# Kernel tuning notes

Measured on AMD Instinct MI355X. Metric: run time of the kernel, lower is better.

Reference implementation:

```python
import jax, jax.numpy as jnp
import numpy as np

NTAPS = 201
N_FWM = 2


def _dw_conv(x, w):
    # depthwise valid cross-correlation: x [N, C, L], w [C, 1, k] -> [N, C, L-k+1]
    return jax.lax.conv_general_dilated(x, w, (1,), 'VALID', feature_group_count=x.shape[1])


def _zcv(x, w):
    # ZcvFilter: x [B, L, Nm] real, w [k]; conv minus center-tap contribution
    B, L, Nm = x.shape
    k = w.shape[0]
    xr = jnp.transpose(x, (0, 2, 1)).reshape(B * Nm, 1, L)
    y = jax.lax.conv_general_dilated(xr, w.reshape(1, 1, k), (1,), 'VALID')
    ov = k - 1
    y = y - w[k // 2] * xr[:, :, ov // 2: L - ov // 2]
    return jnp.transpose(y.reshape(B, Nm, L - k + 1), (0, 2, 1))


def _fwm_filter(x, wr, wi):
    # FwmFilter: x complex [num, B, L, Nm]; depthwise complex conv over L per (num) channel
    num, B, L, Nm = x.shape
    k = wr.shape[-1]
    xp = jnp.transpose(x, (1, 3, 0, 2)).reshape(B * Nm, num, L)  # [B*Nm, num, L]
    yr = _dw_conv(xp.real, wr) - _dw_conv(xp.imag, wi)
    yi = _dw_conv(xp.real, wi) + _dw_conv(xp.imag, wr)
    y = (yr + 1j * yi).reshape(B, Nm, num, L - k + 1)
    return jnp.transpose(y, (2, 0, 3, 1))  # [num, B, L', Nm]


def setup_inputs() -> dict:
    key = jax.random.key(0)
    ks = jax.random.split(key, 8)
    B, M, Nm, k = 16, 40000, 2, NTAPS
    return {
        'x_real': jax.random.normal(ks[0], (B, M, Nm), jnp.float32),
        'x_imag': jax.random.normal(ks[1], (B, M, Nm), jnp.float32),
        'task_info': jax.random.uniform(ks[2], (B, 4), jnp.float32),  # col 0 = power in dBm
        'C00': (jax.random.normal(ks[3], (), jnp.float32) * 0.01),
        'ixpm_w': jax.random.normal(ks[4], (k,), jnp.float32) * 0.01,
        'icixpm_w': jax.random.normal(ks[5], (k,), jnp.float32) * 0.01,
        'fwm_wr': jax.random.normal(ks[6], (2 * N_FWM, 1, k), jnp.float32) * 0.01,
        'fwm_wi': jax.random.normal(ks[7], (2 * N_FWM, 1, k), jnp.float32) * 0.01,
        'i': 0,
    }


def reference(x_real, x_imag, task_info, C00, ixpm_w, icixpm_w, fwm_wr, fwm_wi, i):
    # share=True => module index min(i, 0) == 0; i unused beyond that
    del i
    Nm = x_real.shape[-1]
    t = NTAPS // 2
    P = 10.0 ** (task_info[:, 0] / 10.0) / Nm  # get_power
    sP = jnp.sqrt(P)[:, None, None]
    x = (x_real + 1j * x_imag) * sP  # [B, M, Nm] complex

    def trunc(a):
        return a[:, t:a.shape[1] - t]

    power = jnp.abs(x) ** 2
    ps = 2.0 * power + jnp.roll(power, 1, axis=-1)
    spm = C00 * jnp.sum(trunc(power), axis=-1, keepdims=True)
    ixpm = 2.0 * _zcv(ps, ixpm_w)
    phi = spm + ixpm  # [B, M-ntaps+1, Nm] real

    # FWM branch (n_fwm > 0)
    shifts = [s for s in range(-N_FWM, N_FWM + 1) if s != 0]
    ax = x
    ax_s = jnp.stack([jnp.roll(ax, s, axis=1) for s in shifts])  # [2n, B, M, Nm]
    ay = jnp.roll(x, 1, axis=-1)
    ay_s = jnp.roll(ax_s, 1, axis=-1)
    fwm_A = 2.0 * ax[None] * jnp.conj(ax_s) + ay[None] * jnp.conj(ay_s)
    fwm_B = ax[None] * jnp.conj(ay_s)
    fA = _fwm_filter(fwm_A, fwm_wr, fwm_wi)
    fB = _fwm_filter(fwm_B, fwm_wr, fwm_wi)
    fwm = jnp.sum(ax_s[:, :, t:-t] * fA, axis=0) + jnp.sum(ay_s[:, :, t:-t] * fB, axis=0)

    # icixpm branch
    q = x * jnp.roll(jnp.conj(x), 1, axis=-1)
    qc = _zcv(q.real, icixpm_w) + 1j * _zcv(q.imag, icixpm_w)
    ici = 1j * (jnp.roll(trunc(x), 1, axis=-1) * qc)

    out = trunc(x) * jnp.exp(1j * phi) + ici + fwm
    out = out / sP
    return jnp.stack([out.real, out.imag], axis=-1)  # [B, M-ntaps+1, Nm, 2]
```

## Files before the change

### kernel.cpp

```cpp
#include <hip/hip_runtime.h>
#include <math.h>

#define M_LEN 40000
#define B_SZ 16
#define K_TAPS 201
#define T_HALF 100
#define L_OUT 39800
#define TL 256
#define NTILES 156
#define NP 456
#define NPS 458
#define NPX 460
#define XSTR 464
#define SSTR 244
#define NSER 20
#define KT 7
#define NSLOT 68
#define NTHR 512

typedef unsigned int uint;
typedef unsigned short ushort_;
typedef __fp16 h2 __attribute__((ext_vector_type(2)));
typedef __fp16 h8 __attribute__((ext_vector_type(8)));
typedef float f4 __attribute__((ext_vector_type(4)));

static __device__ __forceinline__ float half_of(uint u, int hi) {
    ushort_ us = hi ? (ushort_)(u >> 16) : (ushort_)(u & 0xffffu);
    _Float16 h; __builtin_memcpy(&h, &us, 2); return (float)h;
}
static __device__ __forceinline__ uint pk2(float a, float b) {
    h2 h = __builtin_amdgcn_cvt_pkrtz(a, b);
    uint r; __builtin_memcpy(&r, &h, 4); return r;
}
static __device__ __forceinline__ h8 mk8(uint a, uint b, uint c, uint d) {
    uint uu[4] = {a, b, c, d}; h8 h; __builtin_memcpy(&h, uu, 16); return h;
}

__global__ void prep_weights(const float* __restrict__ wx, const float* __restrict__ wc,
                             const float* __restrict__ wr, const float* __restrict__ wi,
                             _Float16* __restrict__ Wb) {
    int idx = blockIdx.x * 256 + threadIdx.x;
    if (idx >= 16 * 224) return;
    int n = idx / 224, t = idx % 224;
    float f = 0.f;
    if (n == 0)      f = (t <= 200) ? wx[t] : 0.f;
    else if (n == 1) f = (t <= 200) ? wc[t] : 0.f;
    else if (n < 10) {
        int q = n - 2, sg = q >> 2, c = q & 3;
        if (c < 2) {
            f = (t <= 200) ? ((c == 1) ? wi : wr)[(2 + sg) * K_TAPS + t] : 0.f;
        } else {
            int tt = t - (sg + 1);
            f = (tt >= 0 && tt <= 200) ? ((c == 3) ? wi : wr)[(1 - sg) * K_TAPS + tt] : 0.f;
        }
    }
    Wb[idx] = (_Float16)f;
}

static __device__ __forceinline__ void calc_series(
        const _Float16 (*sxr)[XSTR], const _Float16 (*sxi)[XSTR], int pos, float* v) {
    const int ix = pos + 2;
    float x0r = (float)sxr[0][ix], x0i = (float)sxi[0][ix];
    float x1r = (float)sxr[1][ix], x1i = (float)sxi[1][ix];
    float p0 = x0r * x0r + x0i * x0i;
    float p1 = x1r * x1r + x1i * x1i;
    v[0] = 2.f * p0 + p1;
    v[1] = 2.f * p1 + p0;
    v[2] = x0r * x1r + x0i * x1i;
    v[3] = x0i * x1r - x0r * x1i;
#pragma unroll
    for (int sg = 0; sg < 2; ++sg) {
        const int jx = ix - (sg + 1);
        float a0r = (float)sxr[0][jx], a0i = (float)sxi[0][jx];
        float a1r = (float)sxr[1][jx], a1i = (float)sxi[1][jx];
        float U0r = x0r * a0r + x0i * a0i;
        float U0i = x0i * a0r - x0r * a0i;
        float U1r = x1r * a1r + x1i * a1i;
        float U1i = x1i * a1r - x1r * a1i;
        const int ba = 4 + sg * 8;
        v[ba + 0] = 2.f * U0r + U1r;
        v[ba + 1] = 2.f * U1r + U0r;
        v[ba + 2] = 2.f * U0i + U1i;
        v[ba + 3] = 2.f * U1i + U0i;
        v[ba + 4] = x0r * a1r + x0i * a1i;
        v[ba + 5] = x1r * a0r + x1i * a0i;
        v[ba + 6] = x0i * a1r - x0r * a1i;
        v[ba + 7] = x1i * a0r - x1r * a0i;
    }
}

__global__ __launch_bounds__(NTHR, 4) void snse_kernel(
    const float* __restrict__ g_xr, const float* __restrict__ g_xi,
    const float* __restrict__ g_ti, const float* __restrict__ g_c00,
    const float* __restrict__ g_wx, const float* __restrict__ g_wc,
    const _Float16* __restrict__ Wb,
    float* __restrict__ g_out)
{
    __shared__ uint SEe[NSER * SSTR];
    __shared__ uint SEo[NSER * SSTR];
    __shared__ __align__(16) uint CB2[NSLOT * 128];
    __shared__ _Float16 s_xr_h[2][XSTR], s_xi_h[2][XSTR];

    const int tid = threadIdx.x;
    const int b   = blockIdx.y;
    const int l0  = blockIdx.x * TL;

    const float tdb    = g_ti[b * 4 + 0];
    const float P      = expf(tdb * 0.23025850929940457f) * 0.5f;
    const float sP     = sqrtf(P);
    const float inv_sP = 1.0f / sP;
    const float C00    = g_c00[0];

    for (int idx = tid; idx < 2 * NPX; idx += NTHR) {
        int pidx = idx >> 1, ch = idx & 1;
        int m = l0 - 2 + pidx;
        int mw = m < 0 ? m + M_LEN : (m >= M_LEN ? m - M_LEN : m);
        int gg = (b * M_LEN + mw) * 2 + ch;
        s_xr_h[ch][pidx] = (_Float16)(g_xr[gg] * sP);
        s_xi_h[ch][pidx] = (_Float16)(g_xi[gg] * sP);
    }
    __syncthreads();

    for (int p = tid; p < SSTR; p += NTHR) {
        float v0[NSER], v1[NSER];
#pragma unroll
        for (int a = 0; a < NSER; ++a) { v0[a] = 0.f; v1[a] = 0.f; }
        const int m0 = 2 * p, m1 = 2 * p + 1;
        if (m0 < NPS) calc_series(s_xr_h, s_xi_h, m0, v0);
        if (m1 < NPS) calc_series(s_xr_h, s_xi_h, m1, v1);
#pragma unroll
        for (int a = 0; a < NSER; ++a) {
            _Float16 h0 = (_Float16)v0[a], h1 = (_Float16)v1[a];
            ushort_ s0, s1; __builtin_memcpy(&s0, &h0, 2); __builtin_memcpy(&s1, &h1, 2);
            SEe[a * SSTR + p] = (uint)s0 | ((uint)s1 << 16);
        }
    }
    __syncthreads();

    for (int d = tid; d < NSER * SSTR; d += NTHR) {
        int row = d / SSTR, cc = d - row * SSTR;
        uint lo = SEe[d] >> 16;
        uint hi = (cc < SSTR - 1) ? (SEe[d + 1] << 16) : 0u;
        SEo[d] = lo | hi;
    }
    __syncthreads();

    {
        const int w    = tid >> 6;
        const int lane = tid & 63;
        const int cn   = lane & 15;
        const int gq   = lane >> 4;
        const int rho  = w & 1, hs = (w >> 1) & 1, sgrp = w >> 2;

        h8 Bf[KT];
#pragma unroll
        for (int i = 0; i < KT; ++i) {
            h8 t; __builtin_memcpy(&t, Wb + cn * 224 + 32 * i + 8 * gq, 16);
            Bf[i] = t;
        }

        const uint* SEp = rho ? SEo : SEe;
        const int pbase0 = hs * 128 + rho;
        const int dw0 = ((pbase0 - rho) >> 1) + cn + 4 * gq;
        const int ub0 = rho * 64 + 32 * hs + 2 * gq;

#pragma unroll 1
        for (int as = 0; as < 10; ++as) {
            const int a = sgrp * 10 + as;
            const uint* Pa = SEp + a * SSTR + dw0;

            h8 F[10];
#pragma unroll
            for (int i = 0; i < 10; ++i)
                F[i] = mk8(Pa[16 * i], Pa[16 * i + 1], Pa[16 * i + 2], Pa[16 * i + 3]);

            int slot = -1;
            if (a < 4) {
                if (cn == (a >> 1)) slot = a;
            } else {
                int cb = 2 + 4 * ((a - 4) >> 3);
                int ci = cn - cb;
                if (ci >= 0 && ci < 4) slot = 4 + (a - 4) * 4 + ci;
            }

            f4 Cc[4] = {};
#pragma unroll
            for (int kt = 0; kt < KT; ++kt) {
#pragma unroll
                for (int c = 0; c < 4; ++c)
                    Cc[c] = __builtin_amdgcn_mfma_f32_16x16x32_f16(
                        F[c + kt], Bf[kt], Cc[c], 0, 0, 0);
            }

            if (slot >= 0) {
                const int ub = slot * 128 + ub0;
#pragma unroll
                for (int c = 0; c < 4; ++c) {
                    uint2 v;
                    v.x = pk2(Cc[c][0], Cc[c][1]);
                    v.y = pk2(Cc[c][2], Cc[c][3]);
                    *(uint2*)&CB2[ub + 8 * c] = v;
                }
            }
        }
    }
    __syncthreads();

    {
        const int pos = tid >> 1, nn = tid & 1;
        const int l = l0 + pos;

        const float wx100 = (float)(_Float16)g_wx[T_HALF];
        const float wc100 = (float)(_Float16)g_wc[T_HALF];

        const int par = pos & 1, hp = pos >> 1;
        const int cbb = par * 64 + (hp >> 1);
        const int hl  = hp & 1;

        float acc_ix = half_of(CB2[nn * 128 + cbb], hl);
        float acc_qr = half_of(CB2[2 * 128 + cbb], hl);
        float acc_qi = half_of(CB2[3 * 128 + cbb], hl);

        const int pc = pos + T_HALF;
        acc_ix = fmaf(-wx100, half_of(SEe[nn * SSTR + (pc >> 1)], pc & 1), acc_ix);
        acc_qr = fmaf(-wc100, half_of(SEe[2 * SSTR + (pc >> 1)], pc & 1), acc_qr);
        acc_qi = fmaf(-wc100, half_of(SEe[3 * SSTR + (pc >> 1)], pc & 1), acc_qi);

        float fAr[4], fAi[4], fBr[4], fBi[4];
#pragma unroll
        for (int sg = 0; sg < 2; ++sg) {
            const int sip = 2 + sg, sin_ = 1 - sg;
            const int sb = 4 + 32 * sg;
#define SRD(si, ci) half_of(CB2[(sb + 4 * (si) + (ci)) * 128 + cbb], hl)
            fAr[sip]  = SRD(nn, 0)     - SRD(2 + nn, 1);
            fAi[sip]  = SRD(nn, 1)     + SRD(2 + nn, 0);
            fAr[sin_] = SRD(nn, 2)     + SRD(2 + nn, 3);
            fAi[sin_] = SRD(nn, 3)     - SRD(2 + nn, 2);
            fBr[sip]  = SRD(4 + nn, 0) - SRD(6 + nn, 1);
            fBi[sip]  = SRD(4 + nn, 1) + SRD(6 + nn, 0);
            fBr[sin_] = SRD(5 - nn, 2) + SRD(7 - nn, 3);
            fBi[sin_] = SRD(5 - nn, 3) - SRD(7 - nn, 2);
#undef SRD
        }

        const int xc = pos + T_HALF + 2;
        float X0r = (float)s_xr_h[0][xc], X0i = (float)s_xi_h[0][xc];
        float X1r = (float)s_xr_h[1][xc], X1i = (float)s_xi_h[1][xc];
        float pw  = X0r * X0r + X0i * X0i + X1r * X1r + X1i * X1i;
        float phi = C00 * pw + 2.f * acc_ix;
        float sph, cph;
        __sincosf(phi, &sph, &cph);
        float qcr = acc_qr;
        float qci = nn ? -acc_qi : acc_qi;
        float br_ = nn ? X1r : X0r, bi_ = nn ? X1i : X0i;
        float or_ = nn ? X0r : X1r, oi_ = nn ? X0i : X1i;
        float ici_r = -(or_ * qci + oi_ * qcr);
        float ici_i =   or_ * qcr - oi_ * qci;
        float fw_r = 0.f, fw_i = 0.f;
        const int ssf[4] = {-2, -1, 1, 2};
#pragma unroll
        for (int si = 0; si < 4; ++si) {
            int sx = xc - ssf[si];
            float xnr  = (float)s_xr_h[nn][sx],     xni = (float)s_xi_h[nn][sx];
            float xor_ = (float)s_xr_h[1 - nn][sx], xoi = (float)s_xi_h[1 - nn][sx];
            fw_r += xnr * fAr[si] - xni * fAi[si]
                  + xor_ * fBr[si] - xoi * fBi[si];
            fw_i += xnr * fAi[si] + xni * fAr[si]
                  + xor_ * fBi[si] + xoi * fBr[si];
        }
        float out_r = br_ * cph - bi_ * sph + ici_r + fw_r;
        float out_i = br_ * sph + bi_ * cph + ici_i + fw_i;
        if (l < L_OUT) {
            int oidx = (((b * L_OUT) + l) * 2 + nn) * 2;
            g_out[oidx]     = out_r * inv_sP;
            g_out[oidx + 1] = out_i * inv_sP;
        }
    }
}

extern "C" void kernel_launch(void* const* d_in, const int* in_sizes, int n_in,
                              void* d_out, int out_size, void* d_ws, size_t ws_size,
                              hipStream_t stream) {
    const float* xr  = (const float*)d_in[0];
    const float* xi  = (const float*)d_in[1];
    const float* ti  = (const float*)d_in[2];
    const float* c00 = (const float*)d_in[3];
    const float* wx  = (const float*)d_in[4];
    const float* wc  = (const float*)d_in[5];
    const float* wr  = (const float*)d_in[6];
    const float* wi  = (const float*)d_in[7];
    float* out = (float*)d_out;
    _Float16* Wb = (_Float16*)d_ws;

    prep_weights<<<dim3((16 * 224 + 255) / 256), dim3(256), 0, stream>>>(wx, wc, wr, wi, Wb);

    dim3 grid(NTILES, B_SZ, 1);
    dim3 block(NTHR, 1, 1);
    snse_kernel<<<grid, block, 0, stream>>>(xr, xi, ti, c00, wx, wc, Wb, out);
}
```

Baseline: 168.0 us.

## Halve output tile to 128 and remap MFMA work across waves

Shrinks the per-block output tile from 256 to 128 positions, which cuts shared-memory footprint and lets launch bounds target 6 blocks per CU instead of 4. Each wave now handles 5 series over the full tile rather than 10 over half of it. Operand fragments are reused in a rolling 8-entry register window with a reload between two passes, lowering register pressure. The halo overhead (200 taps of padding per tile) grows relative to useful work, so total LDS staging and series computation per output rises, and half of the threads sit idle in the epilogue.

```diff
diff --git a/kernel.cpp b/kernel.cpp
--- a/kernel.cpp
+++ b/kernel.cpp
@@ -6,15 +6,15 @@
 #define K_TAPS 201
 #define T_HALF 100
 #define L_OUT 39800
-#define TL 256
-#define NTILES 156
-#define NP 456
-#define NPS 458
-#define NPX 460
-#define XSTR 464
-#define SSTR 244
+#define TL 128
+#define NTILES 311
+#define NPS 330
+#define NPX 332
+#define XSTR 336
+#define SSTR 176
 #define NSER 20
 #define KT 7
+#define CBH 72
 #define NSLOT 68
 #define NTHR 512
 
@@ -89,7 +89,7 @@
     }
 }
 
-__global__ __launch_bounds__(NTHR, 4) void snse_kernel(
+__global__ __launch_bounds__(NTHR, 6) void snse_kernel(
     const float* __restrict__ g_xr, const float* __restrict__ g_xi,
     const float* __restrict__ g_ti, const float* __restrict__ g_c00,
     const float* __restrict__ g_wx, const float* __restrict__ g_wc,
@@ -98,7 +98,7 @@
 {
     __shared__ uint SEe[NSER * SSTR];
     __shared__ uint SEo[NSER * SSTR];
-    __shared__ __align__(16) uint CB2[NSLOT * 128];
+    __shared__ __align__(16) uint CB2[NSLOT * CBH];
     __shared__ _Float16 s_xr_h[2][XSTR], s_xi_h[2][XSTR];
 
     const int tid = threadIdx.x;
@@ -129,11 +129,8 @@
         if (m0 < NPS) calc_series(s_xr_h, s_xi_h, m0, v0);
         if (m1 < NPS) calc_series(s_xr_h, s_xi_h, m1, v1);
 #pragma unroll
-        for (int a = 0; a < NSER; ++a) {
-            _Float16 h0 = (_Float16)v0[a], h1 = (_Float16)v1[a];
-            ushort_ s0, s1; __builtin_memcpy(&s0, &h0, 2); __builtin_memcpy(&s1, &h1, 2);
-            SEe[a * SSTR + p] = (uint)s0 | ((uint)s1 << 16);
-        }
+        for (int a = 0; a < NSER; ++a)
+            SEe[a * SSTR + p] = pk2(v0[a], v1[a]);
     }
     __syncthreads();
 
@@ -150,7 +147,7 @@
         const int lane = tid & 63;
         const int cn   = lane & 15;
         const int gq   = lane >> 4;
-        const int rho  = w & 1, hs = (w >> 1) & 1, sgrp = w >> 2;
+        const int rho  = w & 1, sq = w >> 1;
 
         h8 Bf[KT];
 #pragma unroll
@@ -160,19 +157,13 @@
         }
 
         const uint* SEp = rho ? SEo : SEe;
-        const int pbase0 = hs * 128 + rho;
-        const int dw0 = ((pbase0 - rho) >> 1) + cn + 4 * gq;
-        const int ub0 = rho * 64 + 32 * hs + 2 * gq;
+        const int dw0 = cn + 4 * gq;
+        const int ub0 = rho * 32 + 2 * gq;
 
 #pragma unroll 1
-        for (int as = 0; as < 10; ++as) {
-            const int a = sgrp * 10 + as;
+        for (int as = 0; as < 5; ++as) {
+            const int a = 5 * sq + as;
             const uint* Pa = SEp + a * SSTR + dw0;
-
-            h8 F[10];
-#pragma unroll
-            for (int i = 0; i < 10; ++i)
-                F[i] = mk8(Pa[16 * i], Pa[16 * i + 1], Pa[16 * i + 2], Pa[16 * i + 3]);
 
             int slot = -1;
             if (a < 4) {
@@ -183,43 +174,55 @@
                 if (ci >= 0 && ci < 4) slot = 4 + (a - 4) * 4 + ci;
             }
 
-            f4 Cc[4] = {};
-#pragma unroll
-            for (int kt = 0; kt < KT; ++kt) {
-#pragma unroll
-                for (int c = 0; c < 4; ++c)
-                    Cc[c] = __builtin_amdgcn_mfma_f32_16x16x32_f16(
-                        F[c + kt], Bf[kt], Cc[c], 0, 0, 0);
-            }
-
-            if (slot >= 0) {
-                const int ub = slot * 128 + ub0;
-#pragma unroll
-                for (int c = 0; c < 4; ++c) {
-                    uint2 v;
-                    v.x = pk2(Cc[c][0], Cc[c][1]);
-                    v.y = pk2(Cc[c][2], Cc[c][3]);
-                    *(uint2*)&CB2[ub + 8 * c] = v;
+            h8 F[8];
+#pragma unroll
+            for (int i = 0; i < 8; ++i)
+                F[i] = mk8(Pa[16 * i], Pa[16 * i + 1], Pa[16 * i + 2], Pa[16 * i + 3]);
+
+#pragma unroll
+            for (int pr = 0; pr < 2; ++pr) {
+                f4 Cc[2] = {};
+#pragma unroll
+                for (int kt = 0; kt < KT; ++kt) {
+#pragma unroll
+                    for (int cc = 0; cc < 2; ++cc) {
+                        const int c = 2 * pr + cc;
+                        Cc[cc] = __builtin_amdgcn_mfma_f32_16x16x32_f16(
+                            F[(c + kt) & 7], Bf[kt], Cc[cc], 0, 0, 0);
+                    }
+                }
+                if (pr == 0) {
+                    F[0] = mk8(Pa[128], Pa[129], Pa[130], Pa[131]);
+                    F[1] = mk8(Pa[144], Pa[145], Pa[146], Pa[147]);
+                }
+                if (slot >= 0) {
+#pragma unroll
+                    for (int cc = 0; cc < 2; ++cc) {
+                        const int c = 2 * pr + cc;
+                        uint2 v;
+                        v.x = pk2(Cc[cc][0], Cc[cc][1]);
+                        v.y = pk2(Cc[cc][2], Cc[cc][3]);
+                        *(uint2*)&CB2[slot * CBH + ub0 + 8 * c] = v;
+                    }
                 }
             }
         }
     }
     __syncthreads();
 
-    {
+    if (tid < 2 * TL) {
         const int pos = tid >> 1, nn = tid & 1;
         const int l = l0 + pos;
 
         const float wx100 = (float)(_Float16)g_wx[T_HALF];
         const float wc100 = (float)(_Float16)g_wc[T_HALF];
 
-        const int par = pos & 1, hp = pos >> 1;
-        const int cbb = par * 64 + (hp >> 1);
-        const int hl  = hp & 1;
-
-        float acc_ix = half_of(CB2[nn * 128 + cbb], hl);
-        float acc_qr = half_of(CB2[2 * 128 + cbb], hl);
-        float acc_qi = half_of(CB2[3 * 128 + cbb], hl);
+        const int cbb = (pos & 1) * 32 + (pos >> 2);
+        const int hl  = (pos >> 1) & 1;
+
+        float acc_ix = half_of(CB2[nn * CBH + cbb], hl);
+        float acc_qr = half_of(CB2[2 * CBH + cbb], hl);
+        float acc_qi = half_of(CB2[3 * CBH + cbb], hl);
 
         const int pc = pos + T_HALF;
         acc_ix = fmaf(-wx100, half_of(SEe[nn * SSTR + (pc >> 1)], pc & 1), acc_ix);
@@ -231,7 +234,7 @@
         for (int sg = 0; sg < 2; ++sg) {
             const int sip = 2 + sg, sin_ = 1 - sg;
             const int sb = 4 + 32 * sg;
-#define SRD(si, ci) half_of(CB2[(sb + 4 * (si) + (ci)) * 128 + cbb], hl)
+#define SRD(si, ci) half_of(CB2[(sb + 4 * (si) + (ci)) * CBH + cbb], hl)
             fAr[sip]  = SRD(nn, 0)     - SRD(2 + nn, 1);
             fAi[sip]  = SRD(nn, 1)     + SRD(2 + nn, 0);
             fAr[sin_] = SRD(nn, 2)     + SRD(2 + nn, 3);
```

Result: no change. 167.1 us (-0.5%).
